# Kernel tuning notes

Measured on AMD Instinct MI355X. Metric: run time of the kernel, lower is better.

Reference implementation:

```python
import jax, jax.numpy as jnp
import numpy as np

D_MODEL, D_HID, N_HEADS, WIN = 5376, 100, 10, 10
B, T = 8, 4096


def setup_inputs() -> dict:
    key = jax.random.key(0)
    ks = jax.random.split(key, 8)
    x_full = jax.random.normal(ks[0], (B, T, D_MODEL), dtype=jnp.float32)
    lengths = jax.random.randint(ks[1], (B,), T // 4, T + 1)
    mask = jnp.arange(T)[None, :] < lengths[:, None]  # (B,T) bool
    # torch nn.Linear-style params: weight (out,in), bias (out,)
    W1 = jax.random.normal(ks[2], (D_HID, D_MODEL), dtype=jnp.float32) * (1.0 / np.sqrt(D_MODEL))
    b1 = jnp.zeros((D_HID,), dtype=jnp.float32)
    W2 = jax.random.normal(ks[3], (D_HID, D_HID), dtype=jnp.float32) * (1.0 / np.sqrt(D_HID))
    b2 = jnp.zeros((D_HID,), dtype=jnp.float32)
    q = jax.random.normal(ks[4], (N_HEADS, D_HID), dtype=jnp.float32) * 0.02
    v = jax.random.normal(ks[5], (N_HEADS, D_HID), dtype=jnp.float32) * 0.02
    bias = jnp.zeros((), dtype=jnp.float32)
    return {"x_full": x_full, "mask": mask, "W1": W1, "b1": b1,
            "W2": W2, "b2": b2, "q": q, "v": v, "bias": bias}


def reference(x_full, mask, W1, b1, W2, b2, q, v, bias):
    w = WIN
    x = x_full.astype(jnp.float32)
    # TransformMLP: ReLU(W2 @ ReLU(W1 @ x))
    y = jax.nn.relu(jax.nn.relu(x @ W1.T + b1) @ W2.T + b2)  # (B,T,D_HID)
    attn = jnp.einsum('btd,hd->bth', y, q)   # (B,T,H)
    vals = jnp.einsum('btd,hd->bth', y, v)   # (B,T,H)
    Bn, Tn, H = attn.shape
    # left-pad along time by w-1 (pad value irrelevant for attn: those slots have mask=False)
    pa = jnp.pad(attn, ((0, 0), (w - 1, 0), (0, 0)))
    pv = jnp.pad(vals, ((0, 0), (w - 1, 0), (0, 0)))
    pm = jnp.pad(mask, ((0, 0), (w - 1, 0)))
    idx = jnp.arange(Tn)[:, None] + jnp.arange(w)[None, :]  # (T,w) window gather
    wa = pa[:, idx]          # (B,T,w,H)
    wv = pv[:, idx]          # (B,T,w,H)
    wm = pm[:, idx]          # (B,T,w)
    neg_inf = jnp.float32(-jnp.inf)
    wa = jnp.where(wm[..., None], wa, neg_inf)
    all_invalid = ~jnp.any(wm, axis=2)                       # (B,T)
    wa = jnp.where(all_invalid[:, :, None, None], jnp.float32(0.0), wa)
    alpha = jax.nn.softmax(wa, axis=2)                       # over window dim
    alpha = jnp.where(wm[..., None], alpha, jnp.float32(0.0))
    pooled = jnp.sum(alpha * wv, axis=2)                     # (B,T,H)
    pooled = jnp.where(mask[..., None], pooled, neg_inf)
    head_maxes = jnp.max(pooled, axis=1)                     # (B,H)
    return jnp.sum(head_maxes, axis=-1) + bias               # (B,)
```

## Files before the change

kernel.cpp:

```cpp
#include <hip/hip_runtime.h>
#include <stdint.h>

#define D_MODEL 5376
#define D_HID   100
#define NH      10
#define WIN     10
#define BATCH   8
#define TLEN    4096
#define M_TOT   (BATCH*TLEN)
#define KITERS  (D_MODEL/32)
#define BM      64

#define WS_W1P  0
#define WS_W2P  1376256
#define WS_QVP  1409024
#define WS_B1P  1417216
#define WS_B2P  1417728
#define WS_AV   1418240
#define WS_HMAX 5612544

typedef __attribute__((ext_vector_type(8))) short short8;
typedef __attribute__((ext_vector_type(4))) float f32x4;

__device__ __forceinline__ short f2bf(float f) {
    uint32_t u = __float_as_uint(f);
    u += 0x7fff + ((u >> 16) & 1);
    return (short)(u >> 16);
}

__global__ void prep_kernel(const float* __restrict__ W1, const float* __restrict__ b1,
                            const float* __restrict__ W2, const float* __restrict__ b2,
                            const float* __restrict__ q,  const float* __restrict__ v,
                            char* __restrict__ ws) {
    int id = blockIdx.x * 256 + threadIdx.x;
    if (id < 86016) {
        int kb = id >> 9;
        int rem = id & 511;
        int n = rem >> 2, kkb = rem & 3;
        short8 o;
        #pragma unroll
        for (int j = 0; j < 8; j++) {
            int k = kb * 32 + kkb * 8 + j;
            float val = (n < D_HID) ? W1[n * D_MODEL + k] : 0.f;
            o[j] = f2bf(val);
        }
        int off = kb * 8192 + n * 64 + ((kkb ^ ((n >> 1) & 3)) * 16);
        *(short8*)(ws + WS_W1P + off) = o;
    } else if (id < 86016 + 2048) {
        int id2 = id - 86016;
        int kb = id2 >> 9;
        int rem = id2 & 511;
        int n = rem >> 2, kkb = rem & 3;
        short8 o;
        #pragma unroll
        for (int j = 0; j < 8; j++) {
            int k = kb * 32 + kkb * 8 + j;
            float val = (n < D_HID && k < D_HID) ? W2[n * D_HID + k] : 0.f;
            o[j] = f2bf(val);
        }
        int off = kb * 8192 + n * 64 + ((kkb ^ ((n >> 1) & 3)) * 16);
        *(short8*)(ws + WS_W2P + off) = o;
    } else if (id < 86016 + 2048 + 512) {
        int id3 = id - 86016 - 2048;
        int kb = id3 >> 7;
        int rem = id3 & 127;
        int n = rem >> 2, kkb = rem & 3;
        short8 o;
        #pragma unroll
        for (int j = 0; j < 8; j++) {
            int k = kb * 32 + kkb * 8 + j;
            float val = 0.f;
            if (k < D_HID) {
                if (n < NH)            val = q[n * D_HID + k];
                else if (n < 2 * NH)   val = v[(n - NH) * D_HID + k];
            }
            o[j] = f2bf(val);
        }
        int off = kb * 2048 + n * 64 + ((kkb ^ ((n >> 1) & 3)) * 16);
        *(short8*)(ws + WS_QVP + off) = o;
    } else {
        int id4 = id - 86016 - 2048 - 512;
        if (id4 < 128) {
            ((float*)(ws + WS_B1P))[id4] = (id4 < D_HID) ? b1[id4] : 0.f;
        } else if (id4 < 256) {
            int i = id4 - 128;
            ((float*)(ws + WS_B2P))[i] = (i < D_HID) ? b2[i] : 0.f;
        }
    }
}

__global__ __launch_bounds__(256, 2) void mlp_kernel(
    const float* __restrict__ x, const char* __restrict__ W1p,
    const char* __restrict__ W2p, const char* __restrict__ qvp,
    const float* __restrict__ b1p, const float* __restrict__ b2p,
    float* __restrict__ av) {
    __shared__ __align__(16) char smem[34816];
    short* y1 = (short*)smem;
    short* y2 = (short*)(smem + 17408);

    const int tid = threadIdx.x;
    const int w = tid >> 6, lane = tid & 63;
    const int lr = lane & 15, lq = lane >> 4;
    const int blk = blockIdx.x;
    const int rowbase = blk * BM + w * 16;
    const int swz = (lq ^ ((lr >> 1) & 3)) * 16;

    const float* xA = x + (size_t)(rowbase + lr) * D_MODEL + lq * 8;
    const char* gB = W1p + tid * 32;

    f32x4 acc[8];
    #pragma unroll
    for (int i = 0; i < 8; i++) acc[i] = (f32x4)0.f;

    float4 a0 = *(const float4*)(xA);
    float4 a1 = *(const float4*)(xA + 4);
    uint4  s0 = *(const uint4*)(gB);
    uint4  s1 = *(const uint4*)(gB + 16);

    #pragma unroll 2
    for (int i = 0; i < KITERS; i++) {
        char* bb = smem + (i & 1) * 8192;
        *(uint4*)(bb + tid * 32)      = s0;
        *(uint4*)(bb + tid * 32 + 16) = s1;
        short8 afrag;
        afrag[0] = f2bf(a0.x); afrag[1] = f2bf(a0.y);
        afrag[2] = f2bf(a0.z); afrag[3] = f2bf(a0.w);
        afrag[4] = f2bf(a1.x); afrag[5] = f2bf(a1.y);
        afrag[6] = f2bf(a1.z); afrag[7] = f2bf(a1.w);
        __syncthreads();
        if (i + 1 < KITERS) {
            xA += 32; gB += 8192;
            a0 = *(const float4*)(xA);
            a1 = *(const float4*)(xA + 4);
            s0 = *(const uint4*)(gB);
            s1 = *(const uint4*)(gB + 16);
        }
        const char* bbr = smem + (i & 1) * 8192;
        const int baddr = lr * 64 + swz;
        #pragma unroll
        for (int nt = 0; nt < 8; nt++) {
            short8 bfrag = *(const short8*)(bbr + baddr + nt * 1024);
            acc[nt] = __builtin_amdgcn_mfma_f32_16x16x32_bf16(afrag, bfrag, acc[nt], 0, 0, 0);
        }
    }
    __syncthreads();

    #pragma unroll
    for (int nt = 0; nt < 8; nt++) {
        float bias = b1p[nt * 16 + lr];
        #pragma unroll
        for (int r = 0; r < 4; r++) {
            float vv = acc[nt][r] + bias;
            vv = vv > 0.f ? vv : 0.f;
            y1[(w * 16 + lq * 4 + r) * 136 + nt * 16 + lr] = f2bf(vv);
        }
    }
    __syncthreads();

    f32x4 acc2[8];
    #pragma unroll
    for (int i = 0; i < 8; i++) acc2[i] = (f32x4)0.f;
    #pragma unroll
    for (int kt = 0; kt < 4; kt++) {
        short8 a2 = *(const short8*)(y1 + (w * 16 + lr) * 136 + kt * 32 + lq * 8);
        #pragma unroll
        for (int nt = 0; nt < 8; nt++) {
            short8 b2f = *(const short8*)(W2p + kt * 8192 + (nt * 16 + lr) * 64 + swz);
            acc2[nt] = __builtin_amdgcn_mfma_f32_16x16x32_bf16(a2, b2f, acc2[nt], 0, 0, 0);
        }
    }
    #pragma unroll
    for (int nt = 0; nt < 8; nt++) {
        float bias = b2p[nt * 16 + lr];
        #pragma unroll
        for (int r = 0; r < 4; r++) {
            float vv = acc2[nt][r] + bias;
            vv = vv > 0.f ? vv : 0.f;
            y2[(w * 16 + lq * 4 + r) * 136 + nt * 16 + lr] = f2bf(vv);
        }
    }
    __syncthreads();

    f32x4 acc3[2];
    acc3[0] = (f32x4)0.f; acc3[1] = (f32x4)0.f;
    #pragma unroll
    for (int kt = 0; kt < 4; kt++) {
        short8 a3 = *(const short8*)(y2 + (w * 16 + lr) * 136 + kt * 32 + lq * 8);
        #pragma unroll
        for (int nt = 0; nt < 2; nt++) {
            short8 b3f = *(const short8*)(qvp + kt * 2048 + (nt * 16 + lr) * 64 + swz);
            acc3[nt] = __builtin_amdgcn_mfma_f32_16x16x32_bf16(a3, b3f, acc3[nt], 0, 0, 0);
        }
    }
    #pragma unroll
    for (int nt = 0; nt < 2; nt++) {
        #pragma unroll
        for (int r = 0; r < 4; r++) {
            av[(size_t)(rowbase + lq * 4 + r) * 32 + nt * 16 + lr] = acc3[nt][r];
        }
    }
}

__global__ void roll_kernel(const float* __restrict__ av, const void* __restrict__ maskp,
                            float* __restrict__ hmax) {
    const int blk = blockIdx.x;
    const int b = blk / NH, h = blk % NH;
    const unsigned char* mb = (const unsigned char*)maskp;
    const int* mi = (const int*)maskp;
    const bool bytelay = (mb[1] != 0);
    const int tid = threadIdx.x;
    const float* avb = av + (size_t)b * TLEN * 32;
    float lmax = -INFINITY;
    for (int t = tid; t < TLEN; t += 256) {
        bool mt = bytelay ? (mb[b * TLEN + t] != 0) : (mi[b * TLEN + t] != 0);
        if (!mt) continue;
        float wa[WIN], wv[WIN];
        float m = -INFINITY;
        #pragma unroll
        for (int j = 0; j < WIN; j++) {
            int s = t - (WIN - 1) + j;
            bool valid = (s >= 0) &&
                         (bytelay ? (mb[b * TLEN + s] != 0) : (mi[b * TLEN + s] != 0));
            if (valid) { wa[j] = avb[s * 32 + h]; wv[j] = avb[s * 32 + 10 + h]; }
            else       { wa[j] = -INFINITY;       wv[j] = 0.f; }
            m = fmaxf(m, wa[j]);
        }
        float den = 0.f, num = 0.f;
        #pragma unroll
        for (int j = 0; j < WIN; j++) {
            float e = __expf(wa[j] - m);
            den += e;
            num += e * wv[j];
        }
        lmax = fmaxf(lmax, num / den);
    }
    #pragma unroll
    for (int off = 32; off >= 1; off >>= 1)
        lmax = fmaxf(lmax, __shfl_down(lmax, off));
    __shared__ float red[4];
    if ((tid & 63) == 0) red[tid >> 6] = lmax;
    __syncthreads();
    if (tid == 0) {
        hmax[blk] = fmaxf(fmaxf(red[0], red[1]), fmaxf(red[2], red[3]));
    }
}

__global__ void final_kernel(const float* __restrict__ hmax, const float* __restrict__ bias,
                             float* __restrict__ out) {
    int tid = threadIdx.x;
    if (tid < BATCH) {
        float s = bias[0];
        #pragma unroll
        for (int h = 0; h < NH; h++) s += hmax[tid * NH + h];
        out[tid] = s;
    }
}

extern "C" void kernel_launch(void* const* d_in, const int* in_sizes, int n_in,
                              void* d_out, int out_size, void* d_ws, size_t ws_size,
                              hipStream_t stream) {
    const float* x    = (const float*)d_in[0];
    const void*  mask = d_in[1];
    const float* W1   = (const float*)d_in[2];
    const float* b1   = (const float*)d_in[3];
    const float* W2   = (const float*)d_in[4];
    const float* b2   = (const float*)d_in[5];
    const float* q    = (const float*)d_in[6];
    const float* v    = (const float*)d_in[7];
    const float* bias = (const float*)d_in[8];
    char* ws = (char*)d_ws;

    const char*  W1p  = ws + WS_W1P;
    const char*  W2p  = ws + WS_W2P;
    const char*  qvp  = ws + WS_QVP;
    const float* b1p  = (const float*)(ws + WS_B1P);
    const float* b2p  = (const float*)(ws + WS_B2P);
    float*       av   = (float*)(ws + WS_AV);
    float*       hmax = (float*)(ws + WS_HMAX);

    prep_kernel<<<dim3(347), dim3(256), 0, stream>>>(W1, b1, W2, b2, q, v, ws);
    mlp_kernel<<<dim3(M_TOT / BM), dim3(256), 0, stream>>>(x, W1p, W2p, qvp, b1p, b2p, av);
    roll_kernel<<<dim3(BATCH * NH), dim3(256), 0, stream>>>(av, mask, hmax);
    final_kernel<<<dim3(1), dim3(64), 0, stream>>>(hmax, bias, (float*)d_out);
}
```

Measured before the change: 1.005 ms.

## Load W1 fragments directly into registers and drop LDS staging and barriers

The first GEMM no longer stages W1 tiles through shared memory with a block-wide barrier each K step. Each wave now reads its bf16 B fragments straight from global memory into registers, loading the next step's fragments right after each MFMA. The x prefetch becomes two steps deep, alternating between two register buffers. The now-unneeded block barriers after the y1 and y2 shared-memory writes are also removed, since each wave reads back only its own rows. In exchange, every wave fetches the full W1 tile on its own, so W1 traffic through cache rises fourfold, and register pressure goes up.

```diff
diff --git a/kernel.cpp b/kernel.cpp
--- a/kernel.cpp
+++ b/kernel.cpp
@@ -105,45 +105,43 @@
     const int rowbase = blk * BM + w * 16;
     const int swz = (lq ^ ((lr >> 1) & 3)) * 16;
 
-    const float* xA = x + (size_t)(rowbase + lr) * D_MODEL + lq * 8;
-    const char* gB = W1p + tid * 32;
+    const float* xbase = x + (size_t)(rowbase + lr) * D_MODEL + lq * 8;
+    const float* xA = xbase;
+    const char* gB = W1p + lr * 64 + swz;
 
     f32x4 acc[8];
     #pragma unroll
     for (int i = 0; i < 8; i++) acc[i] = (f32x4)0.f;
 
-    float4 a0 = *(const float4*)(xA);
-    float4 a1 = *(const float4*)(xA + 4);
-    uint4  s0 = *(const uint4*)(gB);
-    uint4  s1 = *(const uint4*)(gB + 16);
+    float4 axL[2], axH[2];
+    axL[0] = *(const float4*)(xA);
+    axH[0] = *(const float4*)(xA + 4);
+    axL[1] = *(const float4*)(xA + 32);
+    axH[1] = *(const float4*)(xA + 36);
+    xA += 64;
+    short8 bf[8];
+    #pragma unroll
+    for (int nt = 0; nt < 8; nt++) bf[nt] = *(const short8*)(gB + nt * 1024);
 
     #pragma unroll 2
     for (int i = 0; i < KITERS; i++) {
-        char* bb = smem + (i & 1) * 8192;
-        *(uint4*)(bb + tid * 32)      = s0;
-        *(uint4*)(bb + tid * 32 + 16) = s1;
+        const int par = i & 1;
         short8 afrag;
-        afrag[0] = f2bf(a0.x); afrag[1] = f2bf(a0.y);
-        afrag[2] = f2bf(a0.z); afrag[3] = f2bf(a0.w);
-        afrag[4] = f2bf(a1.x); afrag[5] = f2bf(a1.y);
-        afrag[6] = f2bf(a1.z); afrag[7] = f2bf(a1.w);
-        __syncthreads();
-        if (i + 1 < KITERS) {
-            xA += 32; gB += 8192;
-            a0 = *(const float4*)(xA);
-            a1 = *(const float4*)(xA + 4);
-            s0 = *(const uint4*)(gB);
-            s1 = *(const uint4*)(gB + 16);
-        }
-        const char* bbr = smem + (i & 1) * 8192;
-        const int baddr = lr * 64 + swz;
+        afrag[0] = f2bf(axL[par].x); afrag[1] = f2bf(axL[par].y);
+        afrag[2] = f2bf(axL[par].z); afrag[3] = f2bf(axL[par].w);
+        afrag[4] = f2bf(axH[par].x); afrag[5] = f2bf(axH[par].y);
+        afrag[6] = f2bf(axH[par].z); afrag[7] = f2bf(axH[par].w);
+        const float4* px = (const float4*)((i + 2 < KITERS) ? xA : xbase);
+        axL[par] = px[0];
+        axH[par] = px[1];
+        xA += 32;
+        gB += 8192;
         #pragma unroll
         for (int nt = 0; nt < 8; nt++) {
-            short8 bfrag = *(const short8*)(bbr + baddr + nt * 1024);
-            acc[nt] = __builtin_amdgcn_mfma_f32_16x16x32_bf16(afrag, bfrag, acc[nt], 0, 0, 0);
-        }
-    }
-    __syncthreads();
+            acc[nt] = __builtin_amdgcn_mfma_f32_16x16x32_bf16(afrag, bf[nt], acc[nt], 0, 0, 0);
+            bf[nt] = *(const short8*)(gB + nt * 1024);
+        }
+    }
 
     #pragma unroll
     for (int nt = 0; nt < 8; nt++) {
@@ -155,7 +153,6 @@
             y1[(w * 16 + lq * 4 + r) * 136 + nt * 16 + lr] = f2bf(vv);
         }
     }
-    __syncthreads();
 
     f32x4 acc2[8];
     #pragma unroll
@@ -179,7 +176,6 @@
             y2[(w * 16 + lq * 4 + r) * 136 + nt * 16 + lr] = f2bf(vv);
         }
     }
-    __syncthreads();
 
     f32x4 acc3[2];
     acc3[0] = (f32x4)0.f; acc3[1] = (f32x4)0.f;
```

Result: slower. 1.087 ms (+8.2%).

## Load W1 tiles directly into LDS and split rolling-window pass into chunks

Applied to the files above, without the earlier changes.

The MLP GEMM now stages W1 tiles through global_load_lds (direct global-to-LDS DMA) instead of loading into registers and storing to shared memory, with the barrier moved to the end of each iteration. This is meant to remove VGPR staging and ds_write traffic. Separately, the windowed softmax kernel is split into 16 time chunks per (batch, head), raising the block count from 80 to 1280, and the final kernel now does an extra max reduction over the chunk partials. The risk is in the ordering of the asynchronous LDS loads against the single per-iteration barrier, and the partials buffer must fit in the existing workspace slot.

```diff
diff --git a/kernel.cpp b/kernel.cpp
--- a/kernel.cpp
+++ b/kernel.cpp
@@ -10,6 +10,7 @@
 #define M_TOT   (BATCH*TLEN)
 #define KITERS  (D_MODEL/32)
 #define BM      64
+#define NCHUNK  16
 
 #define WS_W1P  0
 #define WS_W2P  1376256
@@ -26,6 +27,13 @@
     uint32_t u = __float_as_uint(f);
     u += 0x7fff + ((u >> 16) & 1);
     return (short)(u >> 16);
+}
+
+__device__ __forceinline__ void gload_lds16(const char* g, char* l) {
+    __builtin_amdgcn_global_load_lds(
+        (const __attribute__((address_space(1))) void*)g,
+        (__attribute__((address_space(3))) void*)l,
+        16, 0, 0);
 }
 
 __global__ void prep_kernel(const float* __restrict__ W1, const float* __restrict__ b1,
@@ -106,34 +114,33 @@
     const int swz = (lq ^ ((lr >> 1) & 3)) * 16;
 
     const float* xA = x + (size_t)(rowbase + lr) * D_MODEL + lq * 8;
-    const char* gB = W1p + tid * 32;
+    const char* gB0 = W1p + w * 2048 + lane * 16;
 
     f32x4 acc[8];
     #pragma unroll
     for (int i = 0; i < 8; i++) acc[i] = (f32x4)0.f;
 
+    gload_lds16(gB0,        smem + w * 2048);
+    gload_lds16(gB0 + 1024, smem + w * 2048 + 1024);
     float4 a0 = *(const float4*)(xA);
     float4 a1 = *(const float4*)(xA + 4);
-    uint4  s0 = *(const uint4*)(gB);
-    uint4  s1 = *(const uint4*)(gB + 16);
+    __syncthreads();
 
     #pragma unroll 2
     for (int i = 0; i < KITERS; i++) {
-        char* bb = smem + (i & 1) * 8192;
-        *(uint4*)(bb + tid * 32)      = s0;
-        *(uint4*)(bb + tid * 32 + 16) = s1;
         short8 afrag;
         afrag[0] = f2bf(a0.x); afrag[1] = f2bf(a0.y);
         afrag[2] = f2bf(a0.z); afrag[3] = f2bf(a0.w);
         afrag[4] = f2bf(a1.x); afrag[5] = f2bf(a1.y);
         afrag[6] = f2bf(a1.z); afrag[7] = f2bf(a1.w);
-        __syncthreads();
         if (i + 1 < KITERS) {
-            xA += 32; gB += 8192;
+            const char* gBn = gB0 + (i + 1) * 8192;
+            char* lb = smem + ((i + 1) & 1) * 8192 + w * 2048;
+            gload_lds16(gBn,        lb);
+            gload_lds16(gBn + 1024, lb + 1024);
+            xA += 32;
             a0 = *(const float4*)(xA);
             a1 = *(const float4*)(xA + 4);
-            s0 = *(const uint4*)(gB);
-            s1 = *(const uint4*)(gB + 16);
         }
         const char* bbr = smem + (i & 1) * 8192;
         const int baddr = lr * 64 + swz;
@@ -142,8 +149,8 @@
             short8 bfrag = *(const short8*)(bbr + baddr + nt * 1024);
             acc[nt] = __builtin_amdgcn_mfma_f32_16x16x32_bf16(afrag, bfrag, acc[nt], 0, 0, 0);
         }
-    }
-    __syncthreads();
+        __syncthreads();
+    }
 
     #pragma unroll
     for (int nt = 0; nt < 8; nt++) {
@@ -202,18 +209,20 @@
 }
 
 __global__ void roll_kernel(const float* __restrict__ av, const void* __restrict__ maskp,
-                            float* __restrict__ hmax) {
+                            float* __restrict__ hpart) {
     const int blk = blockIdx.x;
-    const int b = blk / NH, h = blk % NH;
+    const int c  = blk & (NCHUNK - 1);
+    const int bh = blk / NCHUNK;
+    const int b = bh / NH, h = bh % NH;
     const unsigned char* mb = (const unsigned char*)maskp;
     const int* mi = (const int*)maskp;
     const bool bytelay = (mb[1] != 0);
     const int tid = threadIdx.x;
     const float* avb = av + (size_t)b * TLEN * 32;
+    const int t = c * (TLEN / NCHUNK) + tid;
     float lmax = -INFINITY;
-    for (int t = tid; t < TLEN; t += 256) {
-        bool mt = bytelay ? (mb[b * TLEN + t] != 0) : (mi[b * TLEN + t] != 0);
-        if (!mt) continue;
+    bool mt = bytelay ? (mb[b * TLEN + t] != 0) : (mi[b * TLEN + t] != 0);
+    if (mt) {
         float wa[WIN], wv[WIN];
         float m = -INFINITY;
         #pragma unroll
@@ -232,7 +241,7 @@
             den += e;
             num += e * wv[j];
         }
-        lmax = fmaxf(lmax, num / den);
+        lmax = num / den;
     }
     #pragma unroll
     for (int off = 32; off >= 1; off >>= 1)
@@ -241,17 +250,25 @@
     if ((tid & 63) == 0) red[tid >> 6] = lmax;
     __syncthreads();
     if (tid == 0) {
-        hmax[blk] = fmaxf(fmaxf(red[0], red[1]), fmaxf(red[2], red[3]));
-    }
-}
-
-__global__ void final_kernel(const float* __restrict__ hmax, const float* __restrict__ bias,
+        hpart[bh * NCHUNK + c] = fmaxf(fmaxf(red[0], red[1]), fmaxf(red[2], red[3]));
+    }
+}
+
+__global__ void final_kernel(const float* __restrict__ hpart, const float* __restrict__ bias,
                              float* __restrict__ out) {
+    __shared__ float red[BATCH * NH];
     int tid = threadIdx.x;
+    if (tid < BATCH * NH) {
+        float m = -INFINITY;
+        #pragma unroll
+        for (int c = 0; c < NCHUNK; c++) m = fmaxf(m, hpart[tid * NCHUNK + c]);
+        red[tid] = m;
+    }
+    __syncthreads();
     if (tid < BATCH) {
         float s = bias[0];
         #pragma unroll
-        for (int h = 0; h < NH; h++) s += hmax[tid * NH + h];
+        for (int h = 0; h < NH; h++) s += red[tid * NH + h];
         out[tid] = s;
     }
 }
@@ -276,10 +293,10 @@
     const float* b1p  = (const float*)(ws + WS_B1P);
     const float* b2p  = (const float*)(ws + WS_B2P);
     float*       av   = (float*)(ws + WS_AV);
-    float*       hmax = (float*)(ws + WS_HMAX);
+    float*       hpart= (float*)(ws + WS_HMAX);
 
     prep_kernel<<<dim3(347), dim3(256), 0, stream>>>(W1, b1, W2, b2, q, v, ws);
     mlp_kernel<<<dim3(M_TOT / BM), dim3(256), 0, stream>>>(x, W1p, W2p, qvp, b1p, b2p, av);
-    roll_kernel<<<dim3(BATCH * NH), dim3(256), 0, stream>>>(av, mask, hmax);
-    final_kernel<<<dim3(1), dim3(64), 0, stream>>>(hmax, bias, (float*)d_out);
-}
+    roll_kernel<<<dim3(BATCH * NH * NCHUNK), dim3(256), 0, stream>>>(av, mask, hpart);
+    final_kernel<<<dim3(1), dim3(128), 0, stream>>>(hpart, bias, (float*)d_out);
+}
```

Result: faster. 945.4 us (-5.9%).
